# Optimization experiments

Measured on AMD Instinct MI355X. Metric: run time of the kernel, lower is better.

## Reference

```python
import jax, jax.numpy as jnp
import numpy as np

N_ATOMS = 16384
N_BLOCKS = 4096
K = 3          # top-k nearest context atoms (min(3, n_ctx) in original; n_ctx >> 3 here)
EPS_W = 1e-8   # inverse-distance weight epsilon (matches original)
EPS_D = 1e-12  # tiny epsilon inside sqrt for numerical safety of the distance


def setup_inputs() -> dict:
    key = jax.random.key(0)
    k1, k2, k3, k4, k5 = jax.random.split(key, 5)
    # coordinates spread out like real molecular coords (Angstrom-ish scale)
    X = jax.random.normal(k1, (N_ATOMS, 3), dtype=jnp.float32) * 10.0
    base_noise = jax.random.normal(k2, (N_ATOMS, 3), dtype=jnp.float32)      # randn_like(X)
    centroid_noise = jax.random.normal(k3, (N_ATOMS, 3), dtype=jnp.float32)  # per-atom randn(3)
    block_ids = jnp.sort(jax.random.randint(k4, (N_ATOMS,), 0, N_BLOCKS)).astype(jnp.int32)
    generate_mask = jax.random.randint(k5, (N_BLOCKS,), 0, 2).astype(bool)
    return {
        "X": X,
        "base_noise": base_noise,
        "centroid_noise": centroid_noise,
        "block_ids": block_ids,
        "generate_mask": generate_mask,
    }


def reference(X, base_noise, centroid_noise, block_ids, generate_mask):
    """Vectorized sample_chemical_prior: for every generated atom, find the 3
    nearest CONTEXT atoms, take an inverse-distance-weighted centroid, and add
    0.5 * gaussian noise. Non-generated atoms keep base_noise (randn_like)."""
    n = X.shape[0]
    gen_atoms = generate_mask[block_ids]           # [N] atoms being generated
    ctx = ~gen_atoms                               # [N] context atoms

    # pairwise squared distances via ||a||^2 + ||b||^2 - 2 a.b  -> [N, N]
    xn = jnp.sum(X * X, axis=-1)
    sq = xn[:, None] + xn[None, :] - 2.0 * (X @ X.T)
    d = jnp.sqrt(jnp.maximum(sq, 0.0) + EPS_D)

    # only context atoms are valid neighbor candidates; exclude self for safety
    not_self = ~jnp.eye(n, dtype=bool)
    d = jnp.where(ctx[None, :] & not_self, d, jnp.inf)

    # k nearest context atoms per row (smallest distances)
    neg_dk, idx = jax.lax.top_k(-d, K)             # [N, K]
    dk = -neg_dk

    # inverse-distance weights, normalized (matches original)
    w = 1.0 / (dk + EPS_W)
    w = w / jnp.sum(w, axis=-1, keepdims=True)

    coords = X[idx]                                # [N, K, 3] gather neighbor coords
    centroid = jnp.sum(coords * w[..., None], axis=1)  # [N, 3]

    x0 = jnp.where(gen_atoms[:, None], centroid + 0.5 * centroid_noise, base_noise)
    return x0
```

## Files before the change

kernel.cpp:

```cpp
#include <hip/hip_runtime.h>
#include <cstdint>

#define N_ATOMS 16384
#define NBLK 64
#define NTHR 256
#define G 24
#define NCELLS 13824
#define NCELLS_PAD 14336
#define CPT 14
#define BOX_LO -48.0f
#define INV_CELL 0.25f
#define SINIT 3.0e38f

#define OFF_COUNTS 0
#define OFF_BLKGEN 256
#define OFF_BLKGOFF 512
#define OFF_FLAGS 1024
#define OFF_ACELL 3072
#define OFF_POS 35840
#define OFF_START 101376
#define OFF_GENIDX 158976
#define OFF_CTX4 224512

__device__ __forceinline__ int cell1(float x) {
    int c = (int)floorf((x - BOX_LO) * INV_CELL);
    return min(max(c, 0), G - 1);
}

__device__ __forceinline__ void ins3(float v, int vi,
                                     float& s1, float& s2, float& s3,
                                     int& i1, int& i2, int& i3)
{
    const bool b1 = v < s1, b2 = v < s2, b3 = v < s3;
    s3 = b2 ? s2 : (b3 ? v : s3);   i3 = b2 ? i2 : (b3 ? vi : i3);
    s2 = b1 ? s1 : (b2 ? v : s2);   i2 = b1 ? i1 : (b2 ? vi : i2);
    s1 = b1 ? v : s1;               i1 = b1 ? vi : i1;
}

__global__ __launch_bounds__(NTHR)
void k1_classify(const float* __restrict__ X,
                 const int* __restrict__ block_ids,
                 const unsigned int* __restrict__ mask,
                 const float* __restrict__ base_noise,
                 float* __restrict__ out,
                 unsigned long long* __restrict__ flags,
                 int* __restrict__ blk_gen,
                 unsigned short* __restrict__ acell)
{
    __shared__ int sflag;
    __shared__ int wg[4];
    const int t = threadIdx.x;
    const int wave = t >> 6, lane = t & 63;

    if (t == 0) sflag = 0;
    __syncthreads();
    if (mask[t] > 1u) sflag = 1;
    __syncthreads();
    const bool is_u8 = (sflag != 0);
    const unsigned char* m8 = (const unsigned char*)mask;

    const int i = blockIdx.x * NTHR + t;
    const int bid = block_ids[i];
    const bool g = is_u8 ? (m8[bid] != 0) : (mask[bid] != 0u);

    out[3 * i + 0] = base_noise[3 * i + 0];
    out[3 * i + 1] = base_noise[3 * i + 1];
    out[3 * i + 2] = base_noise[3 * i + 2];

    const unsigned long long mg = __ballot(g);
    if (lane == 0) { flags[blockIdx.x * 4 + wave] = mg; wg[wave] = __popcll(mg); }
    __syncthreads();
    if (t == 0) blk_gen[blockIdx.x] = wg[0] + wg[1] + wg[2] + wg[3];

    unsigned short c = 0xFFFFu;
    if (!g) {
        const float x = X[3 * i], y = X[3 * i + 1], z = X[3 * i + 2];
        c = (unsigned short)((cell1(z) * G + cell1(y)) * G + cell1(x));
    }
    acell[i] = c;
}

__global__ __launch_bounds__(1024)
void k2_sort(const unsigned short* __restrict__ acell,
             int* __restrict__ cell_start,
             int* __restrict__ pos,
             const int* __restrict__ blk_gen,
             int* __restrict__ blk_goff,
             int* __restrict__ counts)
{
    __shared__ int hist[NCELLS_PAD];
    __shared__ int wsum[16], wexc[16];
    const int t = threadIdx.x;
    const int wave = t >> 6, lane = t & 63;

    #pragma unroll
    for (int k = 0; k < CPT; ++k) hist[t * CPT + k] = 0;
    __syncthreads();

    #pragma unroll
    for (int it = 0; it < N_ATOMS / 1024; ++it) {
        const unsigned short c = acell[it * 1024 + t];
        if (c != 0xFFFFu) atomicAdd(&hist[c], 1);
    }
    __syncthreads();

    int loc[CPT]; int sum = 0;
    #pragma unroll
    for (int k = 0; k < CPT; ++k) {
        const int v = hist[t * CPT + k];
        loc[k] = sum; sum += v;
    }
    int v = sum;
    #pragma unroll
    for (int d = 1; d < 64; d <<= 1) { const int u = __shfl_up(v, d); if (lane >= d) v += u; }
    if (lane == 63) wsum[wave] = v;
    __syncthreads();
    if (t < 16) {
        int v2 = wsum[t];
        const int orig = v2;
        #pragma unroll
        for (int d = 1; d < 16; d <<= 1) { const int u = __shfl_up(v2, d); if (t >= d) v2 += u; }
        wexc[t] = v2 - orig;
    }
    __syncthreads();
    const int base = wexc[wave] + (v - sum);
    #pragma unroll
    for (int k = 0; k < CPT; ++k) {
        const int st = base + loc[k];
        cell_start[t * CPT + k] = st;
        hist[t * CPT + k] = st;
    }
    if (t == 1023) cell_start[NCELLS_PAD] = base + sum;
    __syncthreads();

    #pragma unroll
    for (int it = 0; it < N_ATOMS / 1024; ++it) {
        const int i = it * 1024 + t;
        const unsigned short c = acell[i];
        if (c != 0xFFFFu) pos[i] = atomicAdd(&hist[c], 1);
    }

    if (t < 64) {
        const int o = blk_gen[t];
        int s = o;
        #pragma unroll
        for (int d = 1; d < 64; d <<= 1) { const int u = __shfl_up(s, d); if (t >= d) s += u; }
        blk_goff[t] = s - o;
        if (t == 63) { counts[1] = s; counts[0] = N_ATOMS - s; }
    }
}

__global__ __launch_bounds__(NTHR)
void k3_scatter(const float* __restrict__ X,
                const unsigned long long* __restrict__ flags,
                const int* __restrict__ blk_goff,
                const int* __restrict__ pos,
                float4* __restrict__ ctx4s,
                int* __restrict__ genidx)
{
    const int t = threadIdx.x;
    const int wave = t >> 6, lane = t & 63;
    const int i = blockIdx.x * NTHR + t;
    const unsigned long long fw = flags[blockIdx.x * 4 + wave];
    const bool g = (fw >> lane) & 1ull;
    if (g) {
        int og = blk_goff[blockIdx.x];
        #pragma unroll
        for (int w = 0; w < 4; ++w) {
            if (w < wave) og += __popcll(flags[blockIdx.x * 4 + w]);
        }
        const unsigned long long below = (1ull << lane) - 1ull;
        og += __popcll(fw & below);
        genidx[og] = i;
    } else {
        const float x = X[3 * i], y = X[3 * i + 1], z = X[3 * i + 2];
        float xn = x * x; xn += y * y; xn += z * z;
        ctx4s[pos[i]] = make_float4(x, y, z, xn);
    }
}

__global__ __launch_bounds__(NTHR)
void k4_search(const float* __restrict__ X,
               const float* __restrict__ cnoise,
               const int* __restrict__ counts,
               const int* __restrict__ cell_start,
               const float4* __restrict__ ctx4s,
               const int* __restrict__ genidx,
               float* __restrict__ out)
{
    const int n_gen = counts[1];
    const int wave = threadIdx.x >> 6, lane = threadIdx.x & 63;
    if ((int)blockIdx.x * 4 >= n_gen) return;
    const int slot = (int)blockIdx.x * 4 + wave;
    if (slot >= n_gen) return;

    const int ai = genidx[slot];
    const float qx = X[3 * ai], qy = X[3 * ai + 1], qz = X[3 * ai + 2];
    float xnq = qx * qx; xnq += qy * qy; xnq += qz * qz;
    const int cqx = cell1(qx), cqy = cell1(qy), cqz = cell1(qz);

    float s1 = SINIT, s2 = SINIT, s3 = SINIT;
    int i1 = 0, i2 = 0, i3 = 0;

    {
        int st = 0, cnt = 0;
        if (lane < 9) {
            const int dy = lane % 3 - 1, dz = lane / 3 - 1;
            const int cy = cqy + dy, cz = cqz + dz;
            if ((unsigned)cy < G && (unsigned)cz < G) {
                const int xlo = max(cqx - 1, 0), xhi = min(cqx + 1, G - 1);
                const int c0 = (cz * G + cy) * G + xlo;
                st = cell_start[c0];
                cnt = cell_start[c0 + (xhi - xlo + 1)] - st;
            }
        }
        int stv[9], base[10];
        base[0] = 0;
        #pragma unroll
        for (int k = 0; k < 9; ++k) {
            stv[k] = __builtin_amdgcn_readlane(st, k);
            base[k + 1] = base[k] + __builtin_amdgcn_readlane(cnt, k);
        }
        const int T = base[9];
        const int nro = (T + 63) >> 6;
        if (nro > 0) {
            auto calcP = [&](int j) -> int {
                const int jc = min(j, T - 1);
                int p = stv[0] + jc;
                #pragma unroll
                for (int k = 1; k < 9; ++k)
                    p = (jc >= base[k]) ? stv[k] + (jc - base[k]) : p;
                return p;
            };
            int p0 = calcP(lane);
            float4 cc0 = ctx4s[p0];
            for (int ro = 0; ro < nro; ++ro) {
                int p1 = p0; float4 cc1 = cc0;
                if (ro + 1 < nro) { p1 = calcP((ro + 1) * 64 + lane); cc1 = ctx4s[p1]; }
                if (ro * 64 + lane < T) {
                    const float dot = qx * cc0.x + qy * cc0.y + qz * cc0.z;
                    const float sq = (xnq + cc0.w) - 2.0f * dot;
                    ins3(sq, p0, s1, s2, s3, i1, i2, i3);
                }
                p0 = p1; cc0 = cc1;
            }
        }
    }

    auto converged = [&](float bnd) -> bool {
        const int c = __popcll(__ballot(s1 + 0.01f < bnd))
                    + __popcll(__ballot(s2 + 0.01f < bnd))
                    + __popcll(__ballot(s3 + 0.01f < bnd));
        return c >= 3;
    };

    bool done = converged(16.0f);

    if (!done) {
        auto searchOwner = [&](int ebase_r, int jc) -> int {
            int L = 0;
            #pragma unroll
            for (int stp = 32; stp >= 1; stp >>= 1) {
                const int cand = L + stp;
                const int bv = __shfl(ebase_r, cand);
                if (bv <= jc) L = cand;
            }
            return L;
        };
        auto flatScan = [&](int T, int ebase_r, int pk_r) {
            const int iters = (T + 63) >> 6;
            if (iters == 0) return;
            int jc0 = min(lane, T - 1);
            int p0 = __shfl(pk_r, searchOwner(ebase_r, jc0)) + jc0;
            float4 cc0 = ctx4s[p0];
            for (int it = 0; it < iters; ++it) {
                int p1 = p0; float4 cc1 = cc0;
                if (it + 1 < iters) {
                    const int jc1 = min((it + 1) * 64 + lane, T - 1);
                    p1 = __shfl(pk_r, searchOwner(ebase_r, jc1)) + jc1;
                    cc1 = ctx4s[p1];
                }
                if (it * 64 + lane < T) {
                    const float dot = qx * cc0.x + qy * cc0.y + qz * cc0.z;
                    const float sq = (xnq + cc0.w) - 2.0f * dot;
                    ins3(sq, p0, s1, s2, s3, i1, i2, i3);
                }
                p0 = p1; cc0 = cc1;
            }
        };
        auto prefixT = [&](int cnt, int& ebase_r, int& T) {
            int pre = cnt;
            #pragma unroll
            for (int d = 1; d < 64; d <<= 1) {
                const int u = __shfl_up(pre, d);
                if (lane >= d) pre += u;
            }
            T = __shfl(pre, 63);
            ebase_r = pre - cnt;
        };
        auto ringScan = [&](int P, int R) {
            const int B = 2 * R + 1;
            const int RP = R - P;
            const int PP = 2 * P + 1;
            const int A = 2 * RP * B;
            const int C = PP * 2 * RP;
            const int NS = A + C + 2 * PP * PP;
            auto segRange = [&](int u, int& st, int& cnt) {
                st = 0; cnt = 0;
                if (u >= NS) return;
                int dy, dz, xlo, xhi;
                if (u < A) {
                    const int q = u / B, rdy = u - q * B;
                    dz = (q < RP) ? (-R + q) : (P + 1 + (q - RP));
                    dy = rdy - R;
                    xlo = cqx - R; xhi = cqx + R;
                } else if (u < A + C) {
                    const int v = u - A, W = 2 * RP;
                    const int q = v / W, w = v - q * W;
                    dz = -P + q;
                    dy = (w < RP) ? (-R + w) : (P + 1 + (w - RP));
                    xlo = cqx - R; xhi = cqx + R;
                } else {
                    const int v = u - A - C;
                    const int side = v & 1, v2 = v >> 1;
                    dy = v2 % PP - P; dz = v2 / PP - P;
                    if (side) { xlo = cqx + P + 1; xhi = cqx + R; }
                    else      { xlo = cqx - R;     xhi = cqx - P - 1; }
                }
                const int cy = cqy + dy, cz = cqz + dz;
                if ((unsigned)cy >= G || (unsigned)cz >= G) return;
                xlo = max(xlo, 0); xhi = min(xhi, G - 1);
                if (xlo > xhi) return;
                const int c0 = (cz * G + cy) * G + xlo;
                st = cell_start[c0];
                cnt = cell_start[c0 + (xhi - xlo + 1)] - st;
            };
            const int nro = (NS + 63) >> 6;
            int st0, c0r;
            segRange(lane, st0, c0r);
            for (int ro = 0; ro < nro; ++ro) {
                int st1 = st0, c1r = c0r;
                if (ro + 1 < nro) segRange((ro + 1) * 64 + lane, st1, c1r);
                int eb, Tr;
                prefixT(c0r, eb, Tr);
                if (Tr > 0) flatScan(Tr, eb, st0 - eb);
                st0 = st1; c0r = c1r;
            }
        };

        #pragma unroll
        for (int li = 1; li < 4; ++li) {
            if (!done) {
                const int R = 1 << li;
                ringScan(1 << (li - 1), R);
                done = converged((float)(4 * R) * (float)(4 * R));
            }
        }
        if (!done) {
            s1 = SINIT; s2 = SINIT; s3 = SINIT;
            i1 = 0; i2 = 0; i3 = 0;
            const int n_ctx = counts[0];
            for (int base = 0; base < n_ctx; base += 64) {
                const int p = base + lane;
                if (p < n_ctx) {
                    const float4 cc = ctx4s[p];
                    const float dot = qx * cc.x + qy * cc.y + qz * cc.z;
                    const float sq = (xnq + cc.w) - 2.0f * dot;
                    ins3(sq, p, s1, s2, s3, i1, i2, i3);
                }
            }
        }
    }

    #pragma unroll
    for (int m = 1; m < 64; m <<= 1) {
        const float a = __shfl_xor(s1, m); const int ja = __shfl_xor(i1, m);
        const float b = __shfl_xor(s2, m); const int jb = __shfl_xor(i2, m);
        const float c = __shfl_xor(s3, m); const int jc = __shfl_xor(i3, m);
        ins3(a, ja, s1, s2, s3, i1, i2, i3);
        ins3(b, jb, s1, s2, s3, i1, i2, i3);
        ins3(c, jc, s1, s2, s3, i1, i2, i3);
    }

    if (lane == 0) {
        const float d1 = sqrtf(fmaxf(s1, 0.0f) + 1e-12f);
        const float d2 = sqrtf(fmaxf(s2, 0.0f) + 1e-12f);
        const float d3 = sqrtf(fmaxf(s3, 0.0f) + 1e-12f);
        float w1 = 1.0f / (d1 + 1e-8f);
        float w2 = 1.0f / (d2 + 1e-8f);
        float w3 = 1.0f / (d3 + 1e-8f);
        float wsum = w1 + w2;
        wsum += w3;
        w1 /= wsum; w2 /= wsum; w3 /= wsum;
        const float4 c1 = ctx4s[i1];
        const float4 c2 = ctx4s[i2];
        const float4 c3 = ctx4s[i3];
        float cxo = w1 * c1.x + w2 * c2.x; cxo += w3 * c3.x;
        float cyo = w1 * c1.y + w2 * c2.y; cyo += w3 * c3.y;
        float czo = w1 * c1.z + w2 * c2.z; czo += w3 * c3.z;
        out[3 * ai + 0] = cxo + 0.5f * cnoise[3 * ai + 0];
        out[3 * ai + 1] = cyo + 0.5f * cnoise[3 * ai + 1];
        out[3 * ai + 2] = czo + 0.5f * cnoise[3 * ai + 2];
    }
}

extern "C" void kernel_launch(void* const* d_in, const int* in_sizes, int n_in,
                              void* d_out, int out_size, void* d_ws, size_t ws_size,
                              hipStream_t stream) {
    const float* X          = (const float*)d_in[0];
    const float* base_noise = (const float*)d_in[1];
    const float* cnoise     = (const float*)d_in[2];
    const int*   block_ids  = (const int*)d_in[3];
    const unsigned int* gmask = (const unsigned int*)d_in[4];
    float* out = (float*)d_out;

    char* ws = (char*)d_ws;
    int*    counts     = (int*)(ws + OFF_COUNTS);
    int*    blk_gen    = (int*)(ws + OFF_BLKGEN);
    int*    blk_goff   = (int*)(ws + OFF_BLKGOFF);
    unsigned long long* flags = (unsigned long long*)(ws + OFF_FLAGS);
    unsigned short* acell = (unsigned short*)(ws + OFF_ACELL);
    int*    pos        = (int*)(ws + OFF_POS);
    int*    cell_start = (int*)(ws + OFF_START);
    int*    genidx     = (int*)(ws + OFF_GENIDX);
    float4* ctx4s      = (float4*)(ws + OFF_CTX4);

    k1_classify<<<NBLK, NTHR, 0, stream>>>(X, block_ids, gmask, base_noise,
                                           out, flags, blk_gen, acell);
    k2_sort<<<1, 1024, 0, stream>>>(acell, cell_start, pos, blk_gen, blk_goff, counts);
    k3_scatter<<<NBLK, NTHR, 0, stream>>>(X, flags, blk_goff, pos, ctx4s, genidx);
    k4_search<<<N_ATOMS / 4, NTHR, 0, stream>>>(X, cnoise, counts, cell_start,
                                                ctx4s, genidx, out);
}
```

Measured before the change: 46.01 us.

## Split search into bulk pass and block-cooperative worklist tail pass

The single search kernel becomes two. The first handles queries whose 3x3x3 neighbourhood already gives converged top-3 and pushes unconverged queries to a global worklist via an atomic counter. A second kernel then processes those outliers with a whole 256-thread block per query: ring scans are spread across four waves and the per-wave top-3 results are merged in shared memory. The aim is to remove the wave divergence and long serial tail of a few far queries, at the cost of an extra launch, atomics, and block barriers in the tail kernel.

```diff
diff --git a/kernel.cpp b/kernel.cpp
--- a/kernel.cpp
+++ b/kernel.cpp
@@ -21,6 +21,8 @@
 #define OFF_START 101376
 #define OFF_GENIDX 158976
 #define OFF_CTX4 224512
+#define OFF_WLCNT 486656
+#define OFF_WL 486784
 
 __device__ __forceinline__ int cell1(float x) {
     int c = (int)floorf((x - BOX_LO) * INV_CELL);
@@ -35,6 +37,32 @@
     s3 = b2 ? s2 : (b3 ? v : s3);   i3 = b2 ? i2 : (b3 ? vi : i3);
     s2 = b1 ? s1 : (b2 ? v : s2);   i2 = b1 ? i1 : (b2 ? vi : i2);
     s1 = b1 ? v : s1;               i1 = b1 ? vi : i1;
+}
+
+__device__ __forceinline__ void epilogue(float s1, float s2, float s3,
+                                         int i1, int i2, int i3,
+                                         const float4* __restrict__ ctx4s,
+                                         const float* __restrict__ cnoise,
+                                         float* __restrict__ out, int ai)
+{
+    const float d1 = sqrtf(fmaxf(s1, 0.0f) + 1e-12f);
+    const float d2 = sqrtf(fmaxf(s2, 0.0f) + 1e-12f);
+    const float d3 = sqrtf(fmaxf(s3, 0.0f) + 1e-12f);
+    float w1 = 1.0f / (d1 + 1e-8f);
+    float w2 = 1.0f / (d2 + 1e-8f);
+    float w3 = 1.0f / (d3 + 1e-8f);
+    float wsum = w1 + w2;
+    wsum += w3;
+    w1 /= wsum; w2 /= wsum; w3 /= wsum;
+    const float4 c1 = ctx4s[i1];
+    const float4 c2 = ctx4s[i2];
+    const float4 c3 = ctx4s[i3];
+    float cxo = w1 * c1.x + w2 * c2.x; cxo += w3 * c3.x;
+    float cyo = w1 * c1.y + w2 * c2.y; cyo += w3 * c3.y;
+    float czo = w1 * c1.z + w2 * c2.z; czo += w3 * c3.z;
+    out[3 * ai + 0] = cxo + 0.5f * cnoise[3 * ai + 0];
+    out[3 * ai + 1] = cyo + 0.5f * cnoise[3 * ai + 1];
+    out[3 * ai + 2] = czo + 0.5f * cnoise[3 * ai + 2];
 }
 
 __global__ __launch_bounds__(NTHR)
@@ -45,12 +73,14 @@
                  float* __restrict__ out,
                  unsigned long long* __restrict__ flags,
                  int* __restrict__ blk_gen,
-                 unsigned short* __restrict__ acell)
+                 unsigned short* __restrict__ acell,
+                 int* __restrict__ wl_cnt)
 {
     __shared__ int sflag;
     __shared__ int wg[4];
     const int t = threadIdx.x;
     const int wave = t >> 6, lane = t & 63;
+    if (blockIdx.x == 0 && t == 0) wl_cnt[0] = 0;
 
     if (t == 0) sflag = 0;
     __syncthreads();
@@ -180,13 +210,15 @@
 }
 
 __global__ __launch_bounds__(NTHR)
-void k4_search(const float* __restrict__ X,
-               const float* __restrict__ cnoise,
-               const int* __restrict__ counts,
-               const int* __restrict__ cell_start,
-               const float4* __restrict__ ctx4s,
-               const int* __restrict__ genidx,
-               float* __restrict__ out)
+void k4a_bulk(const float* __restrict__ X,
+              const float* __restrict__ cnoise,
+              const int* __restrict__ counts,
+              const int* __restrict__ cell_start,
+              const float4* __restrict__ ctx4s,
+              const int* __restrict__ genidx,
+              float* __restrict__ out,
+              int* __restrict__ wl_cnt,
+              int* __restrict__ wl)
 {
     const int n_gen = counts[1];
     const int wave = threadIdx.x >> 6, lane = threadIdx.x & 63;
@@ -247,16 +279,54 @@
         }
     }
 
-    auto converged = [&](float bnd) -> bool {
-        const int c = __popcll(__ballot(s1 + 0.01f < bnd))
-                    + __popcll(__ballot(s2 + 0.01f < bnd))
-                    + __popcll(__ballot(s3 + 0.01f < bnd));
-        return c >= 3;
-    };
-
-    bool done = converged(16.0f);
-
-    if (!done) {
+    const int cb = __popcll(__ballot(s1 + 0.01f < 16.0f))
+                 + __popcll(__ballot(s2 + 0.01f < 16.0f))
+                 + __popcll(__ballot(s3 + 0.01f < 16.0f));
+    if (cb < 3) {
+        if (lane == 0) { const int w = atomicAdd(wl_cnt, 1); wl[w] = slot; }
+        return;
+    }
+
+    #pragma unroll
+    for (int m = 1; m < 64; m <<= 1) {
+        const float a = __shfl_xor(s1, m); const int ja = __shfl_xor(i1, m);
+        const float b = __shfl_xor(s2, m); const int jb = __shfl_xor(i2, m);
+        const float c = __shfl_xor(s3, m); const int jc = __shfl_xor(i3, m);
+        ins3(a, ja, s1, s2, s3, i1, i2, i3);
+        ins3(b, jb, s1, s2, s3, i1, i2, i3);
+        ins3(c, jc, s1, s2, s3, i1, i2, i3);
+    }
+    if (lane == 0) epilogue(s1, s2, s3, i1, i2, i3, ctx4s, cnoise, out, ai);
+}
+
+__global__ __launch_bounds__(NTHR)
+void k4b_tail(const float* __restrict__ X,
+              const float* __restrict__ cnoise,
+              const int* __restrict__ counts,
+              const int* __restrict__ cell_start,
+              const float4* __restrict__ ctx4s,
+              const int* __restrict__ genidx,
+              float* __restrict__ out,
+              const int* __restrict__ wl_cnt,
+              const int* __restrict__ wl)
+{
+    __shared__ int cnts[4];
+    __shared__ int dflag;
+    __shared__ int mrg[24];
+    const int t = threadIdx.x;
+    const int wave = t >> 6, lane = t & 63;
+    const int count = wl_cnt[0];
+
+    for (int wid = blockIdx.x; wid < count; wid += gridDim.x) {
+        const int slot = wl[wid];
+        const int ai = genidx[slot];
+        const float qx = X[3 * ai], qy = X[3 * ai + 1], qz = X[3 * ai + 2];
+        float xnq = qx * qx; xnq += qy * qy; xnq += qz * qz;
+        const int cqx = cell1(qx), cqy = cell1(qy), cqz = cell1(qz);
+
+        float s1 = SINIT, s2 = SINIT, s3 = SINIT;
+        int i1 = 0, i2 = 0, i3 = 0;
+
         auto searchOwner = [&](int ebase_r, int jc) -> int {
             int L = 0;
             #pragma unroll
@@ -269,23 +339,16 @@
         };
         auto flatScan = [&](int T, int ebase_r, int pk_r) {
             const int iters = (T + 63) >> 6;
-            if (iters == 0) return;
-            int jc0 = min(lane, T - 1);
-            int p0 = __shfl(pk_r, searchOwner(ebase_r, jc0)) + jc0;
-            float4 cc0 = ctx4s[p0];
             for (int it = 0; it < iters; ++it) {
-                int p1 = p0; float4 cc1 = cc0;
-                if (it + 1 < iters) {
-                    const int jc1 = min((it + 1) * 64 + lane, T - 1);
-                    p1 = __shfl(pk_r, searchOwner(ebase_r, jc1)) + jc1;
-                    cc1 = ctx4s[p1];
+                const int j = it * 64 + lane;
+                const int jc = min(j, T - 1);
+                const int p = __shfl(pk_r, searchOwner(ebase_r, jc)) + jc;
+                const float4 cc = ctx4s[p];
+                if (j < T) {
+                    const float dot = qx * cc.x + qy * cc.y + qz * cc.z;
+                    const float sq = (xnq + cc.w) - 2.0f * dot;
+                    ins3(sq, p, s1, s2, s3, i1, i2, i3);
                 }
-                if (it * 64 + lane < T) {
-                    const float dot = qx * cc0.x + qy * cc0.y + qz * cc0.z;
-                    const float sq = (xnq + cc0.w) - 2.0f * dot;
-                    ins3(sq, p0, s1, s2, s3, i1, i2, i3);
-                }
-                p0 = p1; cc0 = cc1;
             }
         };
         auto prefixT = [&](int cnt, int& ebase_r, int& T) {
@@ -298,70 +361,109 @@
             T = __shfl(pre, 63);
             ebase_r = pre - cnt;
         };
-        auto ringScan = [&](int P, int R) {
-            const int B = 2 * R + 1;
-            const int RP = R - P;
-            const int PP = 2 * P + 1;
-            const int A = 2 * RP * B;
-            const int C = PP * 2 * RP;
-            const int NS = A + C + 2 * PP * PP;
-            auto segRange = [&](int u, int& st, int& cnt) {
-                st = 0; cnt = 0;
-                if (u >= NS) return;
-                int dy, dz, xlo, xhi;
-                if (u < A) {
-                    const int q = u / B, rdy = u - q * B;
-                    dz = (q < RP) ? (-R + q) : (P + 1 + (q - RP));
-                    dy = rdy - R;
-                    xlo = cqx - R; xhi = cqx + R;
-                } else if (u < A + C) {
-                    const int v = u - A, W = 2 * RP;
-                    const int q = v / W, w = v - q * W;
-                    dz = -P + q;
-                    dy = (w < RP) ? (-R + w) : (P + 1 + (w - RP));
-                    xlo = cqx - R; xhi = cqx + R;
-                } else {
-                    const int v = u - A - C;
-                    const int side = v & 1, v2 = v >> 1;
-                    dy = v2 % PP - P; dz = v2 / PP - P;
-                    if (side) { xlo = cqx + P + 1; xhi = cqx + R; }
-                    else      { xlo = cqx - R;     xhi = cqx - P - 1; }
+
+        {
+            int st = 0, cnt = 0;
+            const int ru = wave + 4 * lane;
+            if (lane < 3 && ru < 9) {
+                const int dy = ru % 3 - 1, dz = ru / 3 - 1;
+                const int cy = cqy + dy, cz = cqz + dz;
+                if ((unsigned)cy < G && (unsigned)cz < G) {
+                    const int xlo = max(cqx - 1, 0), xhi = min(cqx + 1, G - 1);
+                    const int c0 = (cz * G + cy) * G + xlo;
+                    st = cell_start[c0];
+                    cnt = cell_start[c0 + (xhi - xlo + 1)] - st;
                 }
-                const int cy = cqy + dy, cz = cqz + dz;
-                if ((unsigned)cy >= G || (unsigned)cz >= G) return;
-                xlo = max(xlo, 0); xhi = min(xhi, G - 1);
-                if (xlo > xhi) return;
-                const int c0 = (cz * G + cy) * G + xlo;
-                st = cell_start[c0];
-                cnt = cell_start[c0 + (xhi - xlo + 1)] - st;
-            };
-            const int nro = (NS + 63) >> 6;
-            int st0, c0r;
-            segRange(lane, st0, c0r);
-            for (int ro = 0; ro < nro; ++ro) {
-                int st1 = st0, c1r = c0r;
-                if (ro + 1 < nro) segRange((ro + 1) * 64 + lane, st1, c1r);
-                int eb, Tr;
-                prefixT(c0r, eb, Tr);
-                if (Tr > 0) flatScan(Tr, eb, st0 - eb);
-                st0 = st1; c0r = c1r;
-            }
+            }
+            int stv[3], base[4];
+            base[0] = 0;
+            #pragma unroll
+            for (int k = 0; k < 3; ++k) {
+                stv[k] = __builtin_amdgcn_readlane(st, k);
+                base[k + 1] = base[k] + __builtin_amdgcn_readlane(cnt, k);
+            }
+            const int T = base[3];
+            for (int j = lane; j < T; j += 64) {
+                int p = stv[0] + j;
+                #pragma unroll
+                for (int k = 1; k < 3; ++k)
+                    p = (j >= base[k]) ? stv[k] + (j - base[k]) : p;
+                const float4 cc = ctx4s[p];
+                const float dot = qx * cc.x + qy * cc.y + qz * cc.z;
+                const float sq = (xnq + cc.w) - 2.0f * dot;
+                ins3(sq, p, s1, s2, s3, i1, i2, i3);
+            }
+        }
+
+        auto blockConv = [&](float bnd) -> bool {
+            const int c = __popcll(__ballot(s1 + 0.01f < bnd))
+                        + __popcll(__ballot(s2 + 0.01f < bnd))
+                        + __popcll(__ballot(s3 + 0.01f < bnd));
+            if (lane == 0) cnts[wave] = c;
+            __syncthreads();
+            if (t == 0) dflag = (cnts[0] + cnts[1] + cnts[2] + cnts[3] >= 3);
+            __syncthreads();
+            return dflag != 0;
         };
 
-        #pragma unroll
+        bool done = blockConv(16.0f);
+
         for (int li = 1; li < 4; ++li) {
             if (!done) {
-                const int R = 1 << li;
-                ringScan(1 << (li - 1), R);
-                done = converged((float)(4 * R) * (float)(4 * R));
+                const int P = 1 << (li - 1), R = 1 << li;
+                const int B = 2 * R + 1;
+                const int RP = R - P;
+                const int PP = 2 * P + 1;
+                const int A = 2 * RP * B;
+                const int C = PP * 2 * RP;
+                const int NS = A + C + 2 * PP * PP;
+                const int nro = (NS + 63) >> 6;
+                for (int ro = wave; ro < nro; ro += 4) {
+                    const int u = ro * 64 + lane;
+                    int st = 0, cnt = 0;
+                    if (u < NS) {
+                        int dy, dz, xlo, xhi;
+                        if (u < A) {
+                            const int q = u / B, rdy = u - q * B;
+                            dz = (q < RP) ? (-R + q) : (P + 1 + (q - RP));
+                            dy = rdy - R;
+                            xlo = cqx - R; xhi = cqx + R;
+                        } else if (u < A + C) {
+                            const int v = u - A, W = 2 * RP;
+                            const int q = v / W, w = v - q * W;
+                            dz = -P + q;
+                            dy = (w < RP) ? (-R + w) : (P + 1 + (w - RP));
+                            xlo = cqx - R; xhi = cqx + R;
+                        } else {
+                            const int v = u - A - C;
+                            const int side = v & 1, v2 = v >> 1;
+                            dy = v2 % PP - P; dz = v2 / PP - P;
+                            if (side) { xlo = cqx + P + 1; xhi = cqx + R; }
+                            else      { xlo = cqx - R;     xhi = cqx - P - 1; }
+                        }
+                        const int cy = cqy + dy, cz = cqz + dz;
+                        if ((unsigned)cy < G && (unsigned)cz < G) {
+                            xlo = max(xlo, 0); xhi = min(xhi, G - 1);
+                            if (xlo <= xhi) {
+                                const int c0 = (cz * G + cy) * G + xlo;
+                                st = cell_start[c0];
+                                cnt = cell_start[c0 + (xhi - xlo + 1)] - st;
+                            }
+                        }
+                    }
+                    int eb, Tr;
+                    prefixT(cnt, eb, Tr);
+                    if (Tr > 0) flatScan(Tr, eb, st - eb);
+                }
+                done = blockConv((float)(4 * R) * (float)(4 * R));
             }
         }
         if (!done) {
             s1 = SINIT; s2 = SINIT; s3 = SINIT;
             i1 = 0; i2 = 0; i3 = 0;
             const int n_ctx = counts[0];
-            for (int base = 0; base < n_ctx; base += 64) {
-                const int p = base + lane;
+            for (int bse = 0; bse < n_ctx; bse += NTHR) {
+                const int p = bse + t;
                 if (p < n_ctx) {
                     const float4 cc = ctx4s[p];
                     const float dot = qx * cc.x + qy * cc.y + qz * cc.z;
@@ -370,37 +472,39 @@
                 }
             }
         }
-    }
-
-    #pragma unroll
-    for (int m = 1; m < 64; m <<= 1) {
-        const float a = __shfl_xor(s1, m); const int ja = __shfl_xor(i1, m);
-        const float b = __shfl_xor(s2, m); const int jb = __shfl_xor(i2, m);
-        const float c = __shfl_xor(s3, m); const int jc = __shfl_xor(i3, m);
-        ins3(a, ja, s1, s2, s3, i1, i2, i3);
-        ins3(b, jb, s1, s2, s3, i1, i2, i3);
-        ins3(c, jc, s1, s2, s3, i1, i2, i3);
-    }
-
-    if (lane == 0) {
-        const float d1 = sqrtf(fmaxf(s1, 0.0f) + 1e-12f);
-        const float d2 = sqrtf(fmaxf(s2, 0.0f) + 1e-12f);
-        const float d3 = sqrtf(fmaxf(s3, 0.0f) + 1e-12f);
-        float w1 = 1.0f / (d1 + 1e-8f);
-        float w2 = 1.0f / (d2 + 1e-8f);
-        float w3 = 1.0f / (d3 + 1e-8f);
-        float wsum = w1 + w2;
-        wsum += w3;
-        w1 /= wsum; w2 /= wsum; w3 /= wsum;
-        const float4 c1 = ctx4s[i1];
-        const float4 c2 = ctx4s[i2];
-        const float4 c3 = ctx4s[i3];
-        float cxo = w1 * c1.x + w2 * c2.x; cxo += w3 * c3.x;
-        float cyo = w1 * c1.y + w2 * c2.y; cyo += w3 * c3.y;
-        float czo = w1 * c1.z + w2 * c2.z; czo += w3 * c3.z;
-        out[3 * ai + 0] = cxo + 0.5f * cnoise[3 * ai + 0];
-        out[3 * ai + 1] = cyo + 0.5f * cnoise[3 * ai + 1];
-        out[3 * ai + 2] = czo + 0.5f * cnoise[3 * ai + 2];
+
+        #pragma unroll
+        for (int m = 1; m < 64; m <<= 1) {
+            const float a = __shfl_xor(s1, m); const int ja = __shfl_xor(i1, m);
+            const float b = __shfl_xor(s2, m); const int jb = __shfl_xor(i2, m);
+            const float c = __shfl_xor(s3, m); const int jc = __shfl_xor(i3, m);
+            ins3(a, ja, s1, s2, s3, i1, i2, i3);
+            ins3(b, jb, s1, s2, s3, i1, i2, i3);
+            ins3(c, jc, s1, s2, s3, i1, i2, i3);
+        }
+        if (lane == 0) {
+            mrg[wave * 6 + 0] = __float_as_int(s1);
+            mrg[wave * 6 + 1] = __float_as_int(s2);
+            mrg[wave * 6 + 2] = __float_as_int(s3);
+            mrg[wave * 6 + 3] = i1;
+            mrg[wave * 6 + 4] = i2;
+            mrg[wave * 6 + 5] = i3;
+        }
+        __syncthreads();
+        if (t == 0) {
+            float a1 = SINIT, a2 = SINIT, a3 = SINIT;
+            int j1 = 0, j2 = 0, j3 = 0;
+            #pragma unroll
+            for (int w = 0; w < 4; ++w) {
+                #pragma unroll
+                for (int k = 0; k < 3; ++k) {
+                    ins3(__int_as_float(mrg[w * 6 + k]), mrg[w * 6 + 3 + k],
+                         a1, a2, a3, j1, j2, j3);
+                }
+            }
+            epilogue(a1, a2, a3, j1, j2, j3, ctx4s, cnoise, out, ai);
+        }
+        __syncthreads();
     }
 }
 
@@ -424,11 +528,15 @@
     int*    cell_start = (int*)(ws + OFF_START);
     int*    genidx     = (int*)(ws + OFF_GENIDX);
     float4* ctx4s      = (float4*)(ws + OFF_CTX4);
+    int*    wl_cnt     = (int*)(ws + OFF_WLCNT);
+    int*    wl         = (int*)(ws + OFF_WL);
 
     k1_classify<<<NBLK, NTHR, 0, stream>>>(X, block_ids, gmask, base_noise,
-                                           out, flags, blk_gen, acell);
+                                           out, flags, blk_gen, acell, wl_cnt);
     k2_sort<<<1, 1024, 0, stream>>>(acell, cell_start, pos, blk_gen, blk_goff, counts);
     k3_scatter<<<NBLK, NTHR, 0, stream>>>(X, flags, blk_goff, pos, ctx4s, genidx);
-    k4_search<<<N_ATOMS / 4, NTHR, 0, stream>>>(X, cnoise, counts, cell_start,
-                                                ctx4s, genidx, out);
-}
+    k4a_bulk<<<N_ATOMS / 4, NTHR, 0, stream>>>(X, cnoise, counts, cell_start,
+                                               ctx4s, genidx, out, wl_cnt, wl);
+    k4b_tail<<<1024, NTHR, 0, stream>>>(X, cnoise, counts, cell_start,
+                                        ctx4s, genidx, out, wl_cnt, wl);
+}
```

After: 54.26 us. +17.9%, slower.

## Fuse scatter into sort kernel and replace ring search with brute-force fallback

Applied to the files above, without the earlier changes.

The separate scatter kernel is folded into the single-block sort kernel: context atoms are written straight to their sorted slot, and generated-atom indices are collected with a shared atomic counter. This removes one launch and the per-block flag and offset bookkeeping, though the order of generated indices now depends on atomic ordering. The multi-ring expanding cell search is also removed. Queries not resolved by the initial neighbourhood now fall back directly to an 8-way unrolled brute-force scan over all context atoms. That cuts code complexity and divergence, but outlier queries that need it become much more expensive.

```diff
diff --git a/kernel.cpp b/kernel.cpp
--- a/kernel.cpp
+++ b/kernel.cpp
@@ -13,14 +13,10 @@
 #define SINIT 3.0e38f
 
 #define OFF_COUNTS 0
-#define OFF_BLKGEN 256
-#define OFF_BLKGOFF 512
-#define OFF_FLAGS 1024
-#define OFF_ACELL 3072
-#define OFF_POS 35840
-#define OFF_START 101376
-#define OFF_GENIDX 158976
-#define OFF_CTX4 224512
+#define OFF_ACELL 256
+#define OFF_START 33280
+#define OFF_GENIDX 90880
+#define OFF_CTX4 156672
 
 __device__ __forceinline__ int cell1(float x) {
     int c = (int)floorf((x - BOX_LO) * INV_CELL);
@@ -43,14 +39,10 @@
                  const unsigned int* __restrict__ mask,
                  const float* __restrict__ base_noise,
                  float* __restrict__ out,
-                 unsigned long long* __restrict__ flags,
-                 int* __restrict__ blk_gen,
                  unsigned short* __restrict__ acell)
 {
     __shared__ int sflag;
-    __shared__ int wg[4];
     const int t = threadIdx.x;
-    const int wave = t >> 6, lane = t & 63;
 
     if (t == 0) sflag = 0;
     __syncthreads();
@@ -66,11 +58,6 @@
     out[3 * i + 0] = base_noise[3 * i + 0];
     out[3 * i + 1] = base_noise[3 * i + 1];
     out[3 * i + 2] = base_noise[3 * i + 2];
-
-    const unsigned long long mg = __ballot(g);
-    if (lane == 0) { flags[blockIdx.x * 4 + wave] = mg; wg[wave] = __popcll(mg); }
-    __syncthreads();
-    if (t == 0) blk_gen[blockIdx.x] = wg[0] + wg[1] + wg[2] + wg[3];
 
     unsigned short c = 0xFFFFu;
     if (!g) {
@@ -81,20 +68,22 @@
 }
 
 __global__ __launch_bounds__(1024)
-void k2_sort(const unsigned short* __restrict__ acell,
-             int* __restrict__ cell_start,
-             int* __restrict__ pos,
-             const int* __restrict__ blk_gen,
-             int* __restrict__ blk_goff,
-             int* __restrict__ counts)
+void k2_sortscatter(const float* __restrict__ X,
+                    const unsigned short* __restrict__ acell,
+                    int* __restrict__ cell_start,
+                    int* __restrict__ counts,
+                    int* __restrict__ genidx,
+                    float4* __restrict__ ctx4s)
 {
     __shared__ int hist[NCELLS_PAD];
     __shared__ int wsum[16], wexc[16];
+    __shared__ int gcnt;
     const int t = threadIdx.x;
     const int wave = t >> 6, lane = t & 63;
 
     #pragma unroll
     for (int k = 0; k < CPT; ++k) hist[t * CPT + k] = 0;
+    if (t == 0) gcnt = 0;
     __syncthreads();
 
     #pragma unroll
@@ -137,46 +126,17 @@
     for (int it = 0; it < N_ATOMS / 1024; ++it) {
         const int i = it * 1024 + t;
         const unsigned short c = acell[i];
-        if (c != 0xFFFFu) pos[i] = atomicAdd(&hist[c], 1);
-    }
-
-    if (t < 64) {
-        const int o = blk_gen[t];
-        int s = o;
-        #pragma unroll
-        for (int d = 1; d < 64; d <<= 1) { const int u = __shfl_up(s, d); if (t >= d) s += u; }
-        blk_goff[t] = s - o;
-        if (t == 63) { counts[1] = s; counts[0] = N_ATOMS - s; }
-    }
-}
-
-__global__ __launch_bounds__(NTHR)
-void k3_scatter(const float* __restrict__ X,
-                const unsigned long long* __restrict__ flags,
-                const int* __restrict__ blk_goff,
-                const int* __restrict__ pos,
-                float4* __restrict__ ctx4s,
-                int* __restrict__ genidx)
-{
-    const int t = threadIdx.x;
-    const int wave = t >> 6, lane = t & 63;
-    const int i = blockIdx.x * NTHR + t;
-    const unsigned long long fw = flags[blockIdx.x * 4 + wave];
-    const bool g = (fw >> lane) & 1ull;
-    if (g) {
-        int og = blk_goff[blockIdx.x];
-        #pragma unroll
-        for (int w = 0; w < 4; ++w) {
-            if (w < wave) og += __popcll(flags[blockIdx.x * 4 + w]);
-        }
-        const unsigned long long below = (1ull << lane) - 1ull;
-        og += __popcll(fw & below);
-        genidx[og] = i;
-    } else {
-        const float x = X[3 * i], y = X[3 * i + 1], z = X[3 * i + 2];
-        float xn = x * x; xn += y * y; xn += z * z;
-        ctx4s[pos[i]] = make_float4(x, y, z, xn);
-    }
+        if (c != 0xFFFFu) {
+            const int p = atomicAdd(&hist[c], 1);
+            const float x = X[3 * i], y = X[3 * i + 1], z = X[3 * i + 2];
+            float xn = x * x; xn += y * y; xn += z * z;
+            ctx4s[p] = make_float4(x, y, z, xn);
+        } else {
+            genidx[atomicAdd(&gcnt, 1)] = i;
+        }
+    }
+    __syncthreads();
+    if (t == 0) { counts[1] = gcnt; counts[0] = N_ATOMS - gcnt; }
 }
 
 __global__ __launch_bounds__(NTHR)
@@ -247,128 +207,37 @@
         }
     }
 
-    auto converged = [&](float bnd) -> bool {
-        const int c = __popcll(__ballot(s1 + 0.01f < bnd))
-                    + __popcll(__ballot(s2 + 0.01f < bnd))
-                    + __popcll(__ballot(s3 + 0.01f < bnd));
-        return c >= 3;
-    };
-
-    bool done = converged(16.0f);
-
-    if (!done) {
-        auto searchOwner = [&](int ebase_r, int jc) -> int {
-            int L = 0;
-            #pragma unroll
-            for (int stp = 32; stp >= 1; stp >>= 1) {
-                const int cand = L + stp;
-                const int bv = __shfl(ebase_r, cand);
-                if (bv <= jc) L = cand;
-            }
-            return L;
-        };
-        auto flatScan = [&](int T, int ebase_r, int pk_r) {
-            const int iters = (T + 63) >> 6;
-            if (iters == 0) return;
-            int jc0 = min(lane, T - 1);
-            int p0 = __shfl(pk_r, searchOwner(ebase_r, jc0)) + jc0;
-            float4 cc0 = ctx4s[p0];
-            for (int it = 0; it < iters; ++it) {
-                int p1 = p0; float4 cc1 = cc0;
-                if (it + 1 < iters) {
-                    const int jc1 = min((it + 1) * 64 + lane, T - 1);
-                    p1 = __shfl(pk_r, searchOwner(ebase_r, jc1)) + jc1;
-                    cc1 = ctx4s[p1];
+    const int cb = __popcll(__ballot(s1 + 0.01f < 16.0f))
+                 + __popcll(__ballot(s2 + 0.01f < 16.0f))
+                 + __popcll(__ballot(s3 + 0.01f < 16.0f));
+
+    if (cb < 3) {
+        s1 = SINIT; s2 = SINIT; s3 = SINIT;
+        i1 = 0; i2 = 0; i3 = 0;
+        const int n_ctx = counts[0];
+        for (int base = 0; base < n_ctx; base += 512) {
+            float4 cv0, cv1, cv2, cv3, cv4, cv5, cv6, cv7;
+            const int pa0 = min(base + 0 * 64 + lane, n_ctx - 1);
+            const int pa1 = min(base + 1 * 64 + lane, n_ctx - 1);
+            const int pa2 = min(base + 2 * 64 + lane, n_ctx - 1);
+            const int pa3 = min(base + 3 * 64 + lane, n_ctx - 1);
+            const int pa4 = min(base + 4 * 64 + lane, n_ctx - 1);
+            const int pa5 = min(base + 5 * 64 + lane, n_ctx - 1);
+            const int pa6 = min(base + 6 * 64 + lane, n_ctx - 1);
+            const int pa7 = min(base + 7 * 64 + lane, n_ctx - 1);
+            cv0 = ctx4s[pa0]; cv1 = ctx4s[pa1]; cv2 = ctx4s[pa2]; cv3 = ctx4s[pa3];
+            cv4 = ctx4s[pa4]; cv5 = ctx4s[pa5]; cv6 = ctx4s[pa6]; cv7 = ctx4s[pa7];
+            #define TAIL_INS(K, CV, PA) \
+                if (base + (K) * 64 + lane < n_ctx) { \
+                    const float dot = qx * (CV).x + qy * (CV).y + qz * (CV).z; \
+                    const float sq = (xnq + (CV).w) - 2.0f * dot; \
+                    ins3(sq, (PA), s1, s2, s3, i1, i2, i3); \
                 }
-                if (it * 64 + lane < T) {
-                    const float dot = qx * cc0.x + qy * cc0.y + qz * cc0.z;
-                    const float sq = (xnq + cc0.w) - 2.0f * dot;
-                    ins3(sq, p0, s1, s2, s3, i1, i2, i3);
-                }
-                p0 = p1; cc0 = cc1;
-            }
-        };
-        auto prefixT = [&](int cnt, int& ebase_r, int& T) {
-            int pre = cnt;
-            #pragma unroll
-            for (int d = 1; d < 64; d <<= 1) {
-                const int u = __shfl_up(pre, d);
-                if (lane >= d) pre += u;
-            }
-            T = __shfl(pre, 63);
-            ebase_r = pre - cnt;
-        };
-        auto ringScan = [&](int P, int R) {
-            const int B = 2 * R + 1;
-            const int RP = R - P;
-            const int PP = 2 * P + 1;
-            const int A = 2 * RP * B;
-            const int C = PP * 2 * RP;
-            const int NS = A + C + 2 * PP * PP;
-            auto segRange = [&](int u, int& st, int& cnt) {
-                st = 0; cnt = 0;
-                if (u >= NS) return;
-                int dy, dz, xlo, xhi;
-                if (u < A) {
-                    const int q = u / B, rdy = u - q * B;
-                    dz = (q < RP) ? (-R + q) : (P + 1 + (q - RP));
-                    dy = rdy - R;
-                    xlo = cqx - R; xhi = cqx + R;
-                } else if (u < A + C) {
-                    const int v = u - A, W = 2 * RP;
-                    const int q = v / W, w = v - q * W;
-                    dz = -P + q;
-                    dy = (w < RP) ? (-R + w) : (P + 1 + (w - RP));
-                    xlo = cqx - R; xhi = cqx + R;
-                } else {
-                    const int v = u - A - C;
-                    const int side = v & 1, v2 = v >> 1;
-                    dy = v2 % PP - P; dz = v2 / PP - P;
-                    if (side) { xlo = cqx + P + 1; xhi = cqx + R; }
-                    else      { xlo = cqx - R;     xhi = cqx - P - 1; }
-                }
-                const int cy = cqy + dy, cz = cqz + dz;
-                if ((unsigned)cy >= G || (unsigned)cz >= G) return;
-                xlo = max(xlo, 0); xhi = min(xhi, G - 1);
-                if (xlo > xhi) return;
-                const int c0 = (cz * G + cy) * G + xlo;
-                st = cell_start[c0];
-                cnt = cell_start[c0 + (xhi - xlo + 1)] - st;
-            };
-            const int nro = (NS + 63) >> 6;
-            int st0, c0r;
-            segRange(lane, st0, c0r);
-            for (int ro = 0; ro < nro; ++ro) {
-                int st1 = st0, c1r = c0r;
-                if (ro + 1 < nro) segRange((ro + 1) * 64 + lane, st1, c1r);
-                int eb, Tr;
-                prefixT(c0r, eb, Tr);
-                if (Tr > 0) flatScan(Tr, eb, st0 - eb);
-                st0 = st1; c0r = c1r;
-            }
-        };
-
-        #pragma unroll
-        for (int li = 1; li < 4; ++li) {
-            if (!done) {
-                const int R = 1 << li;
-                ringScan(1 << (li - 1), R);
-                done = converged((float)(4 * R) * (float)(4 * R));
-            }
-        }
-        if (!done) {
-            s1 = SINIT; s2 = SINIT; s3 = SINIT;
-            i1 = 0; i2 = 0; i3 = 0;
-            const int n_ctx = counts[0];
-            for (int base = 0; base < n_ctx; base += 64) {
-                const int p = base + lane;
-                if (p < n_ctx) {
-                    const float4 cc = ctx4s[p];
-                    const float dot = qx * cc.x + qy * cc.y + qz * cc.z;
-                    const float sq = (xnq + cc.w) - 2.0f * dot;
-                    ins3(sq, p, s1, s2, s3, i1, i2, i3);
-                }
-            }
+            TAIL_INS(0, cv0, pa0) TAIL_INS(1, cv1, pa1)
+            TAIL_INS(2, cv2, pa2) TAIL_INS(3, cv3, pa3)
+            TAIL_INS(4, cv4, pa4) TAIL_INS(5, cv5, pa5)
+            TAIL_INS(6, cv6, pa6) TAIL_INS(7, cv7, pa7)
+            #undef TAIL_INS
         }
     }
 
@@ -416,19 +285,15 @@
 
     char* ws = (char*)d_ws;
     int*    counts     = (int*)(ws + OFF_COUNTS);
-    int*    blk_gen    = (int*)(ws + OFF_BLKGEN);
-    int*    blk_goff   = (int*)(ws + OFF_BLKGOFF);
-    unsigned long long* flags = (unsigned long long*)(ws + OFF_FLAGS);
     unsigned short* acell = (unsigned short*)(ws + OFF_ACELL);
-    int*    pos        = (int*)(ws + OFF_POS);
     int*    cell_start = (int*)(ws + OFF_START);
     int*    genidx     = (int*)(ws + OFF_GENIDX);
     float4* ctx4s      = (float4*)(ws + OFF_CTX4);
 
     k1_classify<<<NBLK, NTHR, 0, stream>>>(X, block_ids, gmask, base_noise,
-                                           out, flags, blk_gen, acell);
-    k2_sort<<<1, 1024, 0, stream>>>(acell, cell_start, pos, blk_gen, blk_goff, counts);
-    k3_scatter<<<NBLK, NTHR, 0, stream>>>(X, flags, blk_goff, pos, ctx4s, genidx);
+                                           out, acell);
+    k2_sortscatter<<<1, 1024, 0, stream>>>(X, acell, cell_start, counts,
+                                           genidx, ctx4s);
     k4_search<<<N_ATOMS / 4, NTHR, 0, stream>>>(X, cnoise, counts, cell_start,
                                                 ctx4s, genidx, out);
 }
```

New measurement: 54.49 us. +18.4%, slower.
